# Optimization experiments

Hardware: AMD Instinct MI355X
Metric: run time of the kernel (lower is better)

Reference implementation:

```python
import jax, jax.numpy as jnp
import numpy as np

N_NODES = 100000
N_EDGES = 1600000
IN_DIM = 128
OUT_DIM = 128
N_HEADS = 4


def setup_inputs() -> dict:
    key = jax.random.key(0)
    k1, k2, k3, k4, k5 = jax.random.split(key, 5)
    h = jax.random.normal(k1, (N_NODES, IN_DIM), dtype=jnp.float32)
    src = jax.random.randint(k2, (N_EDGES,), 0, N_NODES, dtype=jnp.int32)
    dst = jax.random.randint(k3, (N_EDGES,), 0, N_NODES, dtype=jnp.int32)
    s = 1.0 / np.sqrt(IN_DIM)
    W_self = jax.random.normal(k4, (N_HEADS, IN_DIM, OUT_DIM), dtype=jnp.float32) * s
    W_neigh = jax.random.normal(k5, (N_HEADS, IN_DIM, OUT_DIM), dtype=jnp.float32) * s
    b = jnp.zeros((N_HEADS, OUT_DIM), dtype=jnp.float32)
    return {"h": h, "src": src, "dst": dst, "W_self": W_self, "W_neigh": W_neigh, "b": b}


def reference(h, src, dst, W_self, W_neigh, b):
    # Mean neighbor aggregation (shared across heads: SAGEConv 'mean' aggregates
    # raw features, then applies per-head linear layers).
    neigh_sum = jax.ops.segment_sum(h[src], dst, num_segments=N_NODES)   # [N, d_in]
    deg = jax.ops.segment_sum(jnp.ones_like(src, dtype=h.dtype), dst,
                              num_segments=N_NODES)                      # [N]
    h_neigh = neigh_sum / jnp.maximum(deg, 1.0)[:, None]                  # [N, d_in]

    # Per-head: fc_self(h_dst) + fc_neigh(h_neigh) + bias -> [H, N, d_out]
    out = (jnp.einsum('nd,hdo->hno', h, W_self)
           + jnp.einsum('nd,hdo->hno', h_neigh, W_neigh)
           + b[:, None, :])
    # merge='mean': average heads
    return jnp.mean(out, axis=0)  # [N, d_out]
```

## Files before the change

kernel.cpp:

```cpp
#include <hip/hip_runtime.h>

#define N_NODES 100000
#define N_EDGES 1600000
#define DIM 128
#define NH 4

#define NPB 512
#define NB 196
#define CAP 12288
#define BCHUNK 8192
#define BEPT 32
#define NBLK ((N_EDGES + BCHUNK - 1) / BCHUNK)

typedef __attribute__((ext_vector_type(8))) short bf16x8;
typedef __attribute__((ext_vector_type(4))) float f32x4;
typedef __attribute__((ext_vector_type(8))) unsigned short u16x8;

#define B_BCUR   0u
#define B_ROWOFF 4096u
#define B_BBASE  404096u
#define B_CSR    405504u
#define B_WPACK  6805504u
#define B_BAVG   6871040u
#define B_HB     6871552u
#define NEED_BF16 32869376ull

__device__ inline unsigned short f2bf(float x) {
    union { float f; unsigned u; } v; v.f = x;
    unsigned r = v.u + 0x7fffu + ((v.u >> 16) & 1u);
    return (unsigned short)(r >> 16);
}

template <bool BF>
__global__ __launch_bounds__(256) void prep_kernel(
    const float* __restrict__ h, unsigned short* __restrict__ hb,
    const float* __restrict__ Ws, const float* __restrict__ Wn,
    const float* __restrict__ b, unsigned short* __restrict__ wpack,
    float* __restrict__ bavg, int* __restrict__ bcur) {
    const int t = threadIdx.x;
    if (blockIdx.x == 0) bcur[t] = t * CAP;
    int i = blockIdx.x * 256 + t;
    if (i < DIM * DIM) {
        float s = 0.f, n = 0.f;
#pragma unroll
        for (int hh = 0; hh < NH; ++hh) {
            s += Ws[hh * DIM * DIM + i];
            n += Wn[hh * DIM * DIM + i];
        }
        s *= 0.25f; n *= 0.25f;
        int k = i >> 7, o = i & 127;
        int nt = o >> 4, lanelo = o & 15;
        int ks = k >> 5, lanehi = (k & 31) >> 3, e = k & 7;
        int pos = (((nt * 4 + ks) * 64) + lanehi * 16 + lanelo) * 8 + e;
        wpack[pos] = f2bf(s);
        wpack[16384 + pos] = f2bf(n);
    }
    if (i < DIM) {
        float bb = 0.f;
#pragma unroll
        for (int hh = 0; hh < NH; ++hh) bb += b[hh * DIM + i];
        bavg[i] = 0.25f * bb;
    }
    if (BF) {
        const float4* p = reinterpret_cast<const float4*>(h) + (size_t)i * 2;
        float4 a = p[0], c = p[1];
        u16x8 r;
        r[0] = f2bf(a.x); r[1] = f2bf(a.y); r[2] = f2bf(a.z); r[3] = f2bf(a.w);
        r[4] = f2bf(c.x); r[5] = f2bf(c.y); r[6] = f2bf(c.z); r[7] = f2bf(c.w);
        reinterpret_cast<u16x8*>(hb)[i] = r;
    }
}

__global__ __launch_bounds__(256) void bucket_scatter_kernel(const int* __restrict__ src,
                                                             const int* __restrict__ dst,
                                                             int* __restrict__ bcur,
                                                             int* __restrict__ ebuf) {
    __shared__ int stage[BCHUNK];
    __shared__ unsigned char bkt[BCHUNK];
    __shared__ int lc[256], lbase[256], lpos[256];
    int t = threadIdx.x;
    lc[t] = 0;
    lpos[t] = 0;
    __syncthreads();
    int e0 = blockIdx.x * BCHUNK;
#pragma unroll 4
    for (int j = 0; j < BEPT; ++j) {
        int e = e0 + j * 256 + t;
        if (e < N_EDGES) {
            int d = dst[e];
            stage[j * 256 + t] = (src[e] << 9) | (d & (NPB - 1));
            bkt[j * 256 + t] = (unsigned char)(d >> 9);
            atomicAdd(&lc[d >> 9], 1);
        }
    }
    __syncthreads();
    if (lc[t]) lbase[t] = atomicAdd(&bcur[t], lc[t]);
    __syncthreads();
#pragma unroll 4
    for (int j = 0; j < BEPT; ++j) {
        int e = e0 + j * 256 + t;
        if (e < N_EDGES) {
            int bb = bkt[j * 256 + t];
            int o = atomicAdd(&lpos[bb], 1);
            ebuf[lbase[bb] + o] = stage[j * 256 + t];
        }
    }
}

__global__ __launch_bounds__(256) void bucket_scan_kernel(const int* __restrict__ bcur,
                                                          int* __restrict__ bbase) {
    __shared__ int s[256];
    int t = threadIdx.x;
    int v = bcur[t] - t * CAP;
    s[t] = v;
    __syncthreads();
    for (int off = 1; off < 256; off <<= 1) {
        int add = (t >= off) ? s[t - off] : 0;
        __syncthreads();
        s[t] += add;
        __syncthreads();
    }
    bbase[t] = s[t] - v;
}

__global__ __launch_bounds__(256) void csr_build_kernel(const int* __restrict__ bcur,
                                                        const int* __restrict__ bbase,
                                                        const int* __restrict__ ebuf,
                                                        int* __restrict__ rowoff,
                                                        int* __restrict__ csr) {
    __shared__ int h[NPB], off[NPB], cur[NPB], ss[256];
    int b = blockIdx.x, t = threadIdx.x;
    int cnt = bcur[b] - b * CAP;
    int ibase = b * CAP;
    int obase = bbase[b];
    h[t] = 0; h[t + 256] = 0;
    cur[t] = 0; cur[t + 256] = 0;
    __syncthreads();
    for (int i = t; i < cnt; i += 256) atomicAdd(&h[ebuf[ibase + i] & (NPB - 1)], 1);
    __syncthreads();
    int e0 = h[2 * t], e1 = h[2 * t + 1];
    ss[t] = e0 + e1;
    __syncthreads();
    for (int o = 1; o < 256; o <<= 1) {
        int add = (t >= o) ? ss[t - o] : 0;
        __syncthreads();
        ss[t] += add;
        __syncthreads();
    }
    int ex = ss[t] - (e0 + e1);
    off[2 * t] = ex;
    off[2 * t + 1] = ex + e0;
    __syncthreads();
    int n0 = b * NPB;
#pragma unroll
    for (int k = 0; k < 2; ++k) {
        int s2 = 2 * t + k;
        int n = n0 + s2;
        int dg = (k == 0) ? e0 : e1;
        if (n < N_NODES) rowoff[n] = ((obase + off[s2]) << 9) | min(dg, 511);
    }
    for (int i = t; i < cnt; i += 256) {
        int p = ebuf[ibase + i];
        int nl = p & (NPB - 1);
        int o = atomicAdd(&cur[nl], 1);
        csr[obase + off[nl] + o] = p >> 9;
    }
}

template <bool BF>
__global__ __launch_bounds__(256) void gather_mean_kernel(
    const float* __restrict__ h, const unsigned short* __restrict__ hb,
    const int* __restrict__ rowoff, const int* __restrict__ csr,
    float* __restrict__ out) {
    int node = blockIdx.x * 4 + (threadIdx.x >> 6);
    int lane = threadIdx.x & 63;
    int g = lane >> 4;
    int c = lane & 15;
    int w = rowoff[node];
    int lo = w >> 9;
    int dg = w & 511;
    int hi = lo + dg;
    float a0 = 0.f, a1 = 0.f, a2 = 0.f, a3 = 0.f;
    float a4 = 0.f, a5 = 0.f, a6 = 0.f, a7 = 0.f;
    if (BF) {
        int k = lo + g;
        for (; k + 4 < hi; k += 8) {
            int s0 = csr[k], s1 = csr[k + 4];
            uint4 v = *reinterpret_cast<const uint4*>(hb + (size_t)s0 * DIM + c * 8);
            uint4 ww = *reinterpret_cast<const uint4*>(hb + (size_t)s1 * DIM + c * 8);
            a0 += __uint_as_float(v.x << 16) + __uint_as_float(ww.x << 16);
            a1 += __uint_as_float(v.x & 0xffff0000u) + __uint_as_float(ww.x & 0xffff0000u);
            a2 += __uint_as_float(v.y << 16) + __uint_as_float(ww.y << 16);
            a3 += __uint_as_float(v.y & 0xffff0000u) + __uint_as_float(ww.y & 0xffff0000u);
            a4 += __uint_as_float(v.z << 16) + __uint_as_float(ww.z << 16);
            a5 += __uint_as_float(v.z & 0xffff0000u) + __uint_as_float(ww.z & 0xffff0000u);
            a6 += __uint_as_float(v.w << 16) + __uint_as_float(ww.w << 16);
            a7 += __uint_as_float(v.w & 0xffff0000u) + __uint_as_float(ww.w & 0xffff0000u);
        }
        if (k < hi) {
            uint4 v = *reinterpret_cast<const uint4*>(hb + (size_t)csr[k] * DIM + c * 8);
            a0 += __uint_as_float(v.x << 16);
            a1 += __uint_as_float(v.x & 0xffff0000u);
            a2 += __uint_as_float(v.y << 16);
            a3 += __uint_as_float(v.y & 0xffff0000u);
            a4 += __uint_as_float(v.z << 16);
            a5 += __uint_as_float(v.z & 0xffff0000u);
            a6 += __uint_as_float(v.w << 16);
            a7 += __uint_as_float(v.w & 0xffff0000u);
        }
    } else {
        for (int k = lo + g; k < hi; k += 4) {
            int s = csr[k];
            const float4* p = reinterpret_cast<const float4*>(h + (size_t)s * DIM + c * 8);
            float4 x = p[0], y = p[1];
            a0 += x.x; a1 += x.y; a2 += x.z; a3 += x.w;
            a4 += y.x; a5 += y.y; a6 += y.z; a7 += y.w;
        }
    }
    a0 += __shfl_xor(a0, 16, 64); a0 += __shfl_xor(a0, 32, 64);
    a1 += __shfl_xor(a1, 16, 64); a1 += __shfl_xor(a1, 32, 64);
    a2 += __shfl_xor(a2, 16, 64); a2 += __shfl_xor(a2, 32, 64);
    a3 += __shfl_xor(a3, 16, 64); a3 += __shfl_xor(a3, 32, 64);
    a4 += __shfl_xor(a4, 16, 64); a4 += __shfl_xor(a4, 32, 64);
    a5 += __shfl_xor(a5, 16, 64); a5 += __shfl_xor(a5, 32, 64);
    a6 += __shfl_xor(a6, 16, 64); a6 += __shfl_xor(a6, 32, 64);
    a7 += __shfl_xor(a7, 16, 64); a7 += __shfl_xor(a7, 32, 64);
    float inv = 1.0f / (float)max(dg, 1);
    if (g == 0) {
        if (BF) {
            u16x8 r;
            r[0] = f2bf(a0 * inv); r[1] = f2bf(a1 * inv);
            r[2] = f2bf(a2 * inv); r[3] = f2bf(a3 * inv);
            r[4] = f2bf(a4 * inv); r[5] = f2bf(a5 * inv);
            r[6] = f2bf(a6 * inv); r[7] = f2bf(a7 * inv);
            *reinterpret_cast<u16x8*>(reinterpret_cast<unsigned short*>(out) +
                                      (size_t)node * 256 + c * 8) = r;
        } else {
            float4 r0, r1;
            r0.x = a0 * inv; r0.y = a1 * inv; r0.z = a2 * inv; r0.w = a3 * inv;
            r1.x = a4 * inv; r1.y = a5 * inv; r1.z = a6 * inv; r1.w = a7 * inv;
            float4* q = reinterpret_cast<float4*>(out + (size_t)node * DIM + c * 8);
            q[0] = r0;
            q[1] = r1;
        }
    }
}

template <bool BF>
__global__ __launch_bounds__(256) void mfma_gemm_kernel(
    const float* __restrict__ h, const unsigned short* __restrict__ hb,
    float* __restrict__ out, const unsigned short* __restrict__ wpack,
    const float* __restrict__ bavg) {
    const int lane = threadIdx.x & 63;
    const int wid = threadIdx.x >> 6;
    const int node_base = blockIdx.x * 64 + wid * 16;
    const int row = node_base + (lane & 15);
    const int rowc = min(row, N_NODES - 1);
    const int khi = lane >> 4;

    f32x4 acc[8] = {};
    const unsigned short* wn_p = wpack + 16384;

#pragma unroll
    for (int ks = 0; ks < 4; ++ks) {
        const int k0 = ks * 32 + khi * 8;
        bf16x8 ha, na;
        if (BF) {
            ha = *reinterpret_cast<const bf16x8*>(hb + (size_t)rowc * DIM + k0);
            na = *reinterpret_cast<const bf16x8*>(
                reinterpret_cast<const unsigned short*>(out) + (size_t)rowc * 256 + k0);
        } else {
            const float4* hp = reinterpret_cast<const float4*>(h + (size_t)rowc * DIM + k0);
            float4 x = hp[0], y = hp[1];
            ha[0] = (short)f2bf(x.x); ha[1] = (short)f2bf(x.y);
            ha[2] = (short)f2bf(x.z); ha[3] = (short)f2bf(x.w);
            ha[4] = (short)f2bf(y.x); ha[5] = (short)f2bf(y.y);
            ha[6] = (short)f2bf(y.z); ha[7] = (short)f2bf(y.w);
            const float4* np0 = reinterpret_cast<const float4*>(out + (size_t)rowc * DIM + k0);
            float4 u = np0[0], v = np0[1];
            na[0] = (short)f2bf(u.x); na[1] = (short)f2bf(u.y);
            na[2] = (short)f2bf(u.z); na[3] = (short)f2bf(u.w);
            na[4] = (short)f2bf(v.x); na[5] = (short)f2bf(v.y);
            na[6] = (short)f2bf(v.z); na[7] = (short)f2bf(v.w);
        }

#pragma unroll
        for (int nt = 0; nt < 8; ++nt) {
            bf16x8 bs = *reinterpret_cast<const bf16x8*>(wpack + (size_t)(((nt * 4 + ks) * 64 + lane) * 8));
            acc[nt] = __builtin_amdgcn_mfma_f32_16x16x32_bf16(ha, bs, acc[nt], 0, 0, 0);
            bf16x8 bn = *reinterpret_cast<const bf16x8*>(wn_p + (size_t)(((nt * 4 + ks) * 64 + lane) * 8));
            acc[nt] = __builtin_amdgcn_mfma_f32_16x16x32_bf16(na, bn, acc[nt], 0, 0, 0);
        }
    }

    const int r0 = node_base + khi * 4;
#pragma unroll
    for (int nt = 0; nt < 8; ++nt) {
        int o = nt * 16 + (lane & 15);
        float bb = bavg[o];
#pragma unroll
        for (int r = 0; r < 4; ++r) {
            int nr = r0 + r;
            if (nr < N_NODES) out[(size_t)nr * DIM + o] = acc[nt][r] + bb;
        }
    }
}

extern "C" void kernel_launch(void* const* d_in, const int* in_sizes, int n_in,
                              void* d_out, int out_size, void* d_ws, size_t ws_size,
                              hipStream_t stream) {
    const float* h  = (const float*)d_in[0];
    const int* src  = (const int*)d_in[1];
    const int* dst  = (const int*)d_in[2];
    const float* Ws = (const float*)d_in[3];
    const float* Wn = (const float*)d_in[4];
    const float* b  = (const float*)d_in[5];
    float* out = (float*)d_out;

    char* ws = (char*)d_ws;
    int* bcur   = (int*)(ws + B_BCUR);
    int* rowoff = (int*)(ws + B_ROWOFF);
    int* bbase  = (int*)(ws + B_BBASE);
    int* csr    = (int*)(ws + B_CSR);
    unsigned short* wpack = (unsigned short*)(ws + B_WPACK);
    float* bavg = (float*)(ws + B_BAVG);
    unsigned short* hb = (unsigned short*)(ws + B_HB);
    int* ebuf   = (int*)d_out;

    const bool bf = (ws_size >= NEED_BF16);

    if (bf)
        prep_kernel<true><<<(N_NODES * DIM / 8) / 256, 256, 0, stream>>>(h, hb, Ws, Wn, b, wpack, bavg, bcur);
    else
        prep_kernel<false><<<64, 256, 0, stream>>>(h, hb, Ws, Wn, b, wpack, bavg, bcur);
    bucket_scatter_kernel<<<NBLK, 256, 0, stream>>>(src, dst, bcur, ebuf);
    bucket_scan_kernel<<<1, 256, 0, stream>>>(bcur, bbase);
    csr_build_kernel<<<NB, 256, 0, stream>>>(bcur, bbase, ebuf, rowoff, csr);
    if (bf)
        gather_mean_kernel<true><<<N_NODES / 4, 256, 0, stream>>>(h, hb, rowoff, csr, out);
    else
        gather_mean_kernel<false><<<N_NODES / 4, 256, 0, stream>>>(h, hb, rowoff, csr, out);
    const int gemm_blocks = (N_NODES + 63) / 64;
    if (bf)
        mfma_gemm_kernel<true><<<gemm_blocks, 256, 0, stream>>>(h, hb, out, wpack, bavg);
    else
        mfma_gemm_kernel<false><<<gemm_blocks, 256, 0, stream>>>(h, hb, out, wpack, bavg);
}
```

Before: 151.8 us.

## Gather neighbor features in fp8 and fold bucket scan into CSR build

Node features are now stored as fp8 instead of bf16 for the neighbor gather, halving the bytes pulled per edge. Each wave now handles 8 edges in parallel with 16 features per lane. The self-term GEMM input is read from fp32 h and converted to bf16 inside the GEMM. The separate single-block bucket scan kernel is removed, and each CSR block redoes the 256-entry scan itself, saving one launch. The cost is a large precision loss in the aggregated features (fp8 e4m3), which may exceed the tolerance.

```diff
diff --git a/kernel.cpp b/kernel.cpp
--- a/kernel.cpp
+++ b/kernel.cpp
@@ -14,15 +14,15 @@
 
 typedef __attribute__((ext_vector_type(8))) short bf16x8;
 typedef __attribute__((ext_vector_type(4))) float f32x4;
+typedef __attribute__((ext_vector_type(2))) float f32x2;
 typedef __attribute__((ext_vector_type(8))) unsigned short u16x8;
 
 #define B_BCUR   0u
 #define B_ROWOFF 4096u
-#define B_BBASE  404096u
 #define B_CSR    405504u
 #define B_WPACK  6805504u
 #define B_BAVG   6871040u
-#define B_HB     6871552u
+#define B_H8     6871552u
 #define NEED_BF16 32869376ull
 
 __device__ inline unsigned short f2bf(float x) {
@@ -31,9 +31,29 @@
     return (unsigned short)(r >> 16);
 }
 
-template <bool BF>
+__device__ inline void acc_fp8(float (&a)[16], uint4 v) {
+    f32x2 r;
+    r = __builtin_amdgcn_cvt_pk_f32_fp8((int)v.x, false); a[0] += r[0]; a[1] += r[1];
+    r = __builtin_amdgcn_cvt_pk_f32_fp8((int)v.x, true);  a[2] += r[0]; a[3] += r[1];
+    r = __builtin_amdgcn_cvt_pk_f32_fp8((int)v.y, false); a[4] += r[0]; a[5] += r[1];
+    r = __builtin_amdgcn_cvt_pk_f32_fp8((int)v.y, true);  a[6] += r[0]; a[7] += r[1];
+    r = __builtin_amdgcn_cvt_pk_f32_fp8((int)v.z, false); a[8] += r[0]; a[9] += r[1];
+    r = __builtin_amdgcn_cvt_pk_f32_fp8((int)v.z, true);  a[10] += r[0]; a[11] += r[1];
+    r = __builtin_amdgcn_cvt_pk_f32_fp8((int)v.w, false); a[12] += r[0]; a[13] += r[1];
+    r = __builtin_amdgcn_cvt_pk_f32_fp8((int)v.w, true);  a[14] += r[0]; a[15] += r[1];
+}
+
+__device__ inline void acc_f32(float (&a)[16], const float4* p) {
+    float4 x0 = p[0], x1 = p[1], x2 = p[2], x3 = p[3];
+    a[0] += x0.x; a[1] += x0.y; a[2] += x0.z; a[3] += x0.w;
+    a[4] += x1.x; a[5] += x1.y; a[6] += x1.z; a[7] += x1.w;
+    a[8] += x2.x; a[9] += x2.y; a[10] += x2.z; a[11] += x2.w;
+    a[12] += x3.x; a[13] += x3.y; a[14] += x3.z; a[15] += x3.w;
+}
+
+template <bool F8>
 __global__ __launch_bounds__(256) void prep_kernel(
-    const float* __restrict__ h, unsigned short* __restrict__ hb,
+    const float* __restrict__ h, unsigned char* __restrict__ h8,
     const float* __restrict__ Ws, const float* __restrict__ Wn,
     const float* __restrict__ b, unsigned short* __restrict__ wpack,
     float* __restrict__ bavg, int* __restrict__ bcur) {
@@ -61,13 +81,15 @@
         for (int hh = 0; hh < NH; ++hh) bb += b[hh * DIM + i];
         bavg[i] = 0.25f * bb;
     }
-    if (BF) {
+    if (F8) {
         const float4* p = reinterpret_cast<const float4*>(h) + (size_t)i * 2;
         float4 a = p[0], c = p[1];
-        u16x8 r;
-        r[0] = f2bf(a.x); r[1] = f2bf(a.y); r[2] = f2bf(a.z); r[3] = f2bf(a.w);
-        r[4] = f2bf(c.x); r[5] = f2bf(c.y); r[6] = f2bf(c.z); r[7] = f2bf(c.w);
-        reinterpret_cast<u16x8*>(hb)[i] = r;
+        int d0 = 0, d1 = 0;
+        d0 = __builtin_amdgcn_cvt_pk_fp8_f32(a.x, a.y, d0, false);
+        d0 = __builtin_amdgcn_cvt_pk_fp8_f32(a.z, a.w, d0, true);
+        d1 = __builtin_amdgcn_cvt_pk_fp8_f32(c.x, c.y, d1, false);
+        d1 = __builtin_amdgcn_cvt_pk_fp8_f32(c.z, c.w, d1, true);
+        reinterpret_cast<uint2*>(h8)[i] = make_uint2((unsigned)d0, (unsigned)d1);
     }
 }
 
@@ -107,39 +129,15 @@
     }
 }
 
-__global__ __launch_bounds__(256) void bucket_scan_kernel(const int* __restrict__ bcur,
-                                                          int* __restrict__ bbase) {
-    __shared__ int s[256];
-    int t = threadIdx.x;
-    int v = bcur[t] - t * CAP;
-    s[t] = v;
-    __syncthreads();
-    for (int off = 1; off < 256; off <<= 1) {
-        int add = (t >= off) ? s[t - off] : 0;
-        __syncthreads();
-        s[t] += add;
-        __syncthreads();
-    }
-    bbase[t] = s[t] - v;
-}
-
 __global__ __launch_bounds__(256) void csr_build_kernel(const int* __restrict__ bcur,
-                                                        const int* __restrict__ bbase,
                                                         const int* __restrict__ ebuf,
                                                         int* __restrict__ rowoff,
                                                         int* __restrict__ csr) {
-    __shared__ int h[NPB], off[NPB], cur[NPB], ss[256];
+    __shared__ int hh[NPB], off[NPB], cur[NPB], ss[256];
     int b = blockIdx.x, t = threadIdx.x;
     int cnt = bcur[b] - b * CAP;
     int ibase = b * CAP;
-    int obase = bbase[b];
-    h[t] = 0; h[t + 256] = 0;
-    cur[t] = 0; cur[t + 256] = 0;
-    __syncthreads();
-    for (int i = t; i < cnt; i += 256) atomicAdd(&h[ebuf[ibase + i] & (NPB - 1)], 1);
-    __syncthreads();
-    int e0 = h[2 * t], e1 = h[2 * t + 1];
-    ss[t] = e0 + e1;
+    ss[t] = bcur[t] - t * CAP;
     __syncthreads();
     for (int o = 1; o < 256; o <<= 1) {
         int add = (t >= o) ? ss[t - o] : 0;
@@ -147,6 +145,21 @@
         ss[t] += add;
         __syncthreads();
     }
+    int obase = ss[b] - cnt;
+    hh[t] = 0; hh[t + 256] = 0;
+    cur[t] = 0; cur[t + 256] = 0;
+    __syncthreads();
+    for (int i = t; i < cnt; i += 256) atomicAdd(&hh[ebuf[ibase + i] & (NPB - 1)], 1);
+    __syncthreads();
+    int e0 = hh[2 * t], e1 = hh[2 * t + 1];
+    ss[t] = e0 + e1;
+    __syncthreads();
+    for (int o = 1; o < 256; o <<= 1) {
+        int add = (t >= o) ? ss[t - o] : 0;
+        __syncthreads();
+        ss[t] += add;
+        __syncthreads();
+    }
     int ex = ss[t] - (e0 + e1);
     off[2 * t] = ex;
     off[2 * t + 1] = ex + e0;
@@ -156,8 +169,8 @@
     for (int k = 0; k < 2; ++k) {
         int s2 = 2 * t + k;
         int n = n0 + s2;
-        int dg = (k == 0) ? e0 : e1;
-        if (n < N_NODES) rowoff[n] = ((obase + off[s2]) << 9) | min(dg, 511);
+        int dgv = (k == 0) ? e0 : e1;
+        if (n < N_NODES) rowoff[n] = ((obase + off[s2]) << 9) | min(dgv, 511);
     }
     for (int i = t; i < cnt; i += 256) {
         int p = ebuf[ibase + i];
@@ -167,90 +180,69 @@
     }
 }
 
-template <bool BF>
+template <bool F8>
 __global__ __launch_bounds__(256) void gather_mean_kernel(
-    const float* __restrict__ h, const unsigned short* __restrict__ hb,
+    const float* __restrict__ h, const unsigned char* __restrict__ h8,
     const int* __restrict__ rowoff, const int* __restrict__ csr,
     float* __restrict__ out) {
-    int node = blockIdx.x * 4 + (threadIdx.x >> 6);
-    int lane = threadIdx.x & 63;
-    int g = lane >> 4;
-    int c = lane & 15;
-    int w = rowoff[node];
-    int lo = w >> 9;
-    int dg = w & 511;
-    int hi = lo + dg;
-    float a0 = 0.f, a1 = 0.f, a2 = 0.f, a3 = 0.f;
-    float a4 = 0.f, a5 = 0.f, a6 = 0.f, a7 = 0.f;
-    if (BF) {
-        int k = lo + g;
-        for (; k + 4 < hi; k += 8) {
-            int s0 = csr[k], s1 = csr[k + 4];
-            uint4 v = *reinterpret_cast<const uint4*>(hb + (size_t)s0 * DIM + c * 8);
-            uint4 ww = *reinterpret_cast<const uint4*>(hb + (size_t)s1 * DIM + c * 8);
-            a0 += __uint_as_float(v.x << 16) + __uint_as_float(ww.x << 16);
-            a1 += __uint_as_float(v.x & 0xffff0000u) + __uint_as_float(ww.x & 0xffff0000u);
-            a2 += __uint_as_float(v.y << 16) + __uint_as_float(ww.y << 16);
-            a3 += __uint_as_float(v.y & 0xffff0000u) + __uint_as_float(ww.y & 0xffff0000u);
-            a4 += __uint_as_float(v.z << 16) + __uint_as_float(ww.z << 16);
-            a5 += __uint_as_float(v.z & 0xffff0000u) + __uint_as_float(ww.z & 0xffff0000u);
-            a6 += __uint_as_float(v.w << 16) + __uint_as_float(ww.w << 16);
-            a7 += __uint_as_float(v.w & 0xffff0000u) + __uint_as_float(ww.w & 0xffff0000u);
-        }
-        if (k < hi) {
-            uint4 v = *reinterpret_cast<const uint4*>(hb + (size_t)csr[k] * DIM + c * 8);
-            a0 += __uint_as_float(v.x << 16);
-            a1 += __uint_as_float(v.x & 0xffff0000u);
-            a2 += __uint_as_float(v.y << 16);
-            a3 += __uint_as_float(v.y & 0xffff0000u);
-            a4 += __uint_as_float(v.z << 16);
-            a5 += __uint_as_float(v.z & 0xffff0000u);
-            a6 += __uint_as_float(v.w << 16);
-            a7 += __uint_as_float(v.w & 0xffff0000u);
+    const int node = blockIdx.x * 4 + (threadIdx.x >> 6);
+    const int lane = threadIdx.x & 63;
+    const int s = lane >> 3;
+    const int c = lane & 7;
+    const int w = rowoff[node];
+    const int lo = w >> 9, dg = w & 511, hi = lo + dg;
+    float a[16];
+#pragma unroll
+    for (int i = 0; i < 16; ++i) a[i] = 0.f;
+    if (F8 && dg >= 8) {
+        int k = lo + s;
+        for (; k + 8 < hi; k += 16) {
+            int s0 = csr[k], s1 = csr[k + 8];
+            uint4 v = *reinterpret_cast<const uint4*>(h8 + (size_t)s0 * DIM + c * 16);
+            uint4 u = *reinterpret_cast<const uint4*>(h8 + (size_t)s1 * DIM + c * 16);
+            acc_fp8(a, v);
+            acc_fp8(a, u);
+        }
+        for (; k < hi; k += 8) {
+            uint4 v = *reinterpret_cast<const uint4*>(h8 + (size_t)csr[k] * DIM + c * 16);
+            acc_fp8(a, v);
         }
     } else {
-        for (int k = lo + g; k < hi; k += 4) {
-            int s = csr[k];
-            const float4* p = reinterpret_cast<const float4*>(h + (size_t)s * DIM + c * 8);
-            float4 x = p[0], y = p[1];
-            a0 += x.x; a1 += x.y; a2 += x.z; a3 += x.w;
-            a4 += y.x; a5 += y.y; a6 += y.z; a7 += y.w;
-        }
-    }
-    a0 += __shfl_xor(a0, 16, 64); a0 += __shfl_xor(a0, 32, 64);
-    a1 += __shfl_xor(a1, 16, 64); a1 += __shfl_xor(a1, 32, 64);
-    a2 += __shfl_xor(a2, 16, 64); a2 += __shfl_xor(a2, 32, 64);
-    a3 += __shfl_xor(a3, 16, 64); a3 += __shfl_xor(a3, 32, 64);
-    a4 += __shfl_xor(a4, 16, 64); a4 += __shfl_xor(a4, 32, 64);
-    a5 += __shfl_xor(a5, 16, 64); a5 += __shfl_xor(a5, 32, 64);
-    a6 += __shfl_xor(a6, 16, 64); a6 += __shfl_xor(a6, 32, 64);
-    a7 += __shfl_xor(a7, 16, 64); a7 += __shfl_xor(a7, 32, 64);
+        for (int k = lo + s; k < hi; k += 8)
+            acc_f32(a, reinterpret_cast<const float4*>(h + (size_t)csr[k] * DIM + c * 16));
+    }
+#pragma unroll
+    for (int i = 0; i < 16; ++i) {
+        a[i] += __shfl_xor(a[i], 8, 64);
+        a[i] += __shfl_xor(a[i], 16, 64);
+        a[i] += __shfl_xor(a[i], 32, 64);
+    }
     float inv = 1.0f / (float)max(dg, 1);
-    if (g == 0) {
-        if (BF) {
-            u16x8 r;
-            r[0] = f2bf(a0 * inv); r[1] = f2bf(a1 * inv);
-            r[2] = f2bf(a2 * inv); r[3] = f2bf(a3 * inv);
-            r[4] = f2bf(a4 * inv); r[5] = f2bf(a5 * inv);
-            r[6] = f2bf(a6 * inv); r[7] = f2bf(a7 * inv);
-            *reinterpret_cast<u16x8*>(reinterpret_cast<unsigned short*>(out) +
-                                      (size_t)node * 256 + c * 8) = r;
+    if (s == 0) {
+        if (F8) {
+            u16x8 r0, r1;
+#pragma unroll
+            for (int j = 0; j < 8; ++j) {
+                r0[j] = f2bf(a[j] * inv);
+                r1[j] = f2bf(a[8 + j] * inv);
+            }
+            unsigned short* base = reinterpret_cast<unsigned short*>(out) + (size_t)node * 256 + c * 16;
+            *reinterpret_cast<u16x8*>(base) = r0;
+            *reinterpret_cast<u16x8*>(base + 8) = r1;
         } else {
-            float4 r0, r1;
-            r0.x = a0 * inv; r0.y = a1 * inv; r0.z = a2 * inv; r0.w = a3 * inv;
-            r1.x = a4 * inv; r1.y = a5 * inv; r1.z = a6 * inv; r1.w = a7 * inv;
-            float4* q = reinterpret_cast<float4*>(out + (size_t)node * DIM + c * 8);
-            q[0] = r0;
-            q[1] = r1;
-        }
-    }
-}
-
-template <bool BF>
+            float4* q = reinterpret_cast<float4*>(out + (size_t)node * DIM + c * 16);
+            q[0] = make_float4(a[0] * inv, a[1] * inv, a[2] * inv, a[3] * inv);
+            q[1] = make_float4(a[4] * inv, a[5] * inv, a[6] * inv, a[7] * inv);
+            q[2] = make_float4(a[8] * inv, a[9] * inv, a[10] * inv, a[11] * inv);
+            q[3] = make_float4(a[12] * inv, a[13] * inv, a[14] * inv, a[15] * inv);
+        }
+    }
+}
+
+template <bool F8>
 __global__ __launch_bounds__(256) void mfma_gemm_kernel(
-    const float* __restrict__ h, const unsigned short* __restrict__ hb,
-    float* __restrict__ out, const unsigned short* __restrict__ wpack,
-    const float* __restrict__ bavg) {
+    const float* __restrict__ h, float* __restrict__ out,
+    const unsigned short* __restrict__ wpack, const float* __restrict__ bavg) {
     const int lane = threadIdx.x & 63;
     const int wid = threadIdx.x >> 6;
     const int node_base = blockIdx.x * 64 + wid * 16;
@@ -265,17 +257,16 @@
     for (int ks = 0; ks < 4; ++ks) {
         const int k0 = ks * 32 + khi * 8;
         bf16x8 ha, na;
-        if (BF) {
-            ha = *reinterpret_cast<const bf16x8*>(hb + (size_t)rowc * DIM + k0);
+        const float4* hp = reinterpret_cast<const float4*>(h + (size_t)rowc * DIM + k0);
+        float4 x = hp[0], y = hp[1];
+        ha[0] = (short)f2bf(x.x); ha[1] = (short)f2bf(x.y);
+        ha[2] = (short)f2bf(x.z); ha[3] = (short)f2bf(x.w);
+        ha[4] = (short)f2bf(y.x); ha[5] = (short)f2bf(y.y);
+        ha[6] = (short)f2bf(y.z); ha[7] = (short)f2bf(y.w);
+        if (F8) {
             na = *reinterpret_cast<const bf16x8*>(
                 reinterpret_cast<const unsigned short*>(out) + (size_t)rowc * 256 + k0);
         } else {
-            const float4* hp = reinterpret_cast<const float4*>(h + (size_t)rowc * DIM + k0);
-            float4 x = hp[0], y = hp[1];
-            ha[0] = (short)f2bf(x.x); ha[1] = (short)f2bf(x.y);
-            ha[2] = (short)f2bf(x.z); ha[3] = (short)f2bf(x.w);
-            ha[4] = (short)f2bf(y.x); ha[5] = (short)f2bf(y.y);
-            ha[6] = (short)f2bf(y.z); ha[7] = (short)f2bf(y.w);
             const float4* np0 = reinterpret_cast<const float4*>(out + (size_t)rowc * DIM + k0);
             float4 u = np0[0], v = np0[1];
             na[0] = (short)f2bf(u.x); na[1] = (short)f2bf(u.y);
@@ -320,29 +311,27 @@
     char* ws = (char*)d_ws;
     int* bcur   = (int*)(ws + B_BCUR);
     int* rowoff = (int*)(ws + B_ROWOFF);
-    int* bbase  = (int*)(ws + B_BBASE);
     int* csr    = (int*)(ws + B_CSR);
     unsigned short* wpack = (unsigned short*)(ws + B_WPACK);
     float* bavg = (float*)(ws + B_BAVG);
-    unsigned short* hb = (unsigned short*)(ws + B_HB);
+    unsigned char* h8 = (unsigned char*)(ws + B_H8);
     int* ebuf   = (int*)d_out;
 
-    const bool bf = (ws_size >= NEED_BF16);
-
-    if (bf)
-        prep_kernel<true><<<(N_NODES * DIM / 8) / 256, 256, 0, stream>>>(h, hb, Ws, Wn, b, wpack, bavg, bcur);
+    const bool f8 = (ws_size >= NEED_BF16);
+
+    if (f8)
+        prep_kernel<true><<<(N_NODES * DIM / 8) / 256, 256, 0, stream>>>(h, h8, Ws, Wn, b, wpack, bavg, bcur);
     else
-        prep_kernel<false><<<64, 256, 0, stream>>>(h, hb, Ws, Wn, b, wpack, bavg, bcur);
+        prep_kernel<false><<<64, 256, 0, stream>>>(h, h8, Ws, Wn, b, wpack, bavg, bcur);
     bucket_scatter_kernel<<<NBLK, 256, 0, stream>>>(src, dst, bcur, ebuf);
-    bucket_scan_kernel<<<1, 256, 0, stream>>>(bcur, bbase);
-    csr_build_kernel<<<NB, 256, 0, stream>>>(bcur, bbase, ebuf, rowoff, csr);
-    if (bf)
-        gather_mean_kernel<true><<<N_NODES / 4, 256, 0, stream>>>(h, hb, rowoff, csr, out);
+    csr_build_kernel<<<NB, 256, 0, stream>>>(bcur, ebuf, rowoff, csr);
+    if (f8)
+        gather_mean_kernel<true><<<N_NODES / 4, 256, 0, stream>>>(h, h8, rowoff, csr, out);
     else
-        gather_mean_kernel<false><<<N_NODES / 4, 256, 0, stream>>>(h, hb, rowoff, csr, out);
+        gather_mean_kernel<false><<<N_NODES / 4, 256, 0, stream>>>(h, h8, rowoff, csr, out);
     const int gemm_blocks = (N_NODES + 63) / 64;
-    if (bf)
-        mfma_gemm_kernel<true><<<gemm_blocks, 256, 0, stream>>>(h, hb, out, wpack, bavg);
+    if (f8)
+        mfma_gemm_kernel<true><<<gemm_blocks, 256, 0, stream>>>(h, out, wpack, bavg);
     else
-        mfma_gemm_kernel<false><<<gemm_blocks, 256, 0, stream>>>(h, hb, out, wpack, bavg);
-}
+        mfma_gemm_kernel<false><<<gemm_blocks, 256, 0, stream>>>(h, out, wpack, bavg);
+}
```

Measured after the change: 146.8 us. 3.3% less time.

## Fuse neighbor gather-mean with MFMA GEMM and fold bucket scan into CSR build

Applied to the files above, without the earlier changes.

The neighbor mean aggregation and the per-node MFMA GEMM are merged into one kernel. Each 1024-thread block gathers 16 nodes into LDS as bf16, then 8 waves each compute one 16-column output tile. This removes the global round-trip of the aggregated features and one kernel launch. The separate single-block bucket scan is also removed: every CSR-build block redundantly recomputes the 256-entry prefix sum itself. In exchange, half the waves sit idle during the GEMM phase, the W fragments are reloaded per block, and the large blocks may limit occupancy.

```diff
diff --git a/kernel.cpp b/kernel.cpp
--- a/kernel.cpp
+++ b/kernel.cpp
@@ -18,7 +18,6 @@
 
 #define B_BCUR   0u
 #define B_ROWOFF 4096u
-#define B_BBASE  404096u
 #define B_CSR    405504u
 #define B_WPACK  6805504u
 #define B_BAVG   6871040u
@@ -107,39 +106,15 @@
     }
 }
 
-__global__ __launch_bounds__(256) void bucket_scan_kernel(const int* __restrict__ bcur,
-                                                          int* __restrict__ bbase) {
-    __shared__ int s[256];
-    int t = threadIdx.x;
-    int v = bcur[t] - t * CAP;
-    s[t] = v;
-    __syncthreads();
-    for (int off = 1; off < 256; off <<= 1) {
-        int add = (t >= off) ? s[t - off] : 0;
-        __syncthreads();
-        s[t] += add;
-        __syncthreads();
-    }
-    bbase[t] = s[t] - v;
-}
-
 __global__ __launch_bounds__(256) void csr_build_kernel(const int* __restrict__ bcur,
-                                                        const int* __restrict__ bbase,
                                                         const int* __restrict__ ebuf,
                                                         int* __restrict__ rowoff,
                                                         int* __restrict__ csr) {
-    __shared__ int h[NPB], off[NPB], cur[NPB], ss[256];
+    __shared__ int hh[NPB], off[NPB], cur[NPB], ss[256];
     int b = blockIdx.x, t = threadIdx.x;
     int cnt = bcur[b] - b * CAP;
     int ibase = b * CAP;
-    int obase = bbase[b];
-    h[t] = 0; h[t + 256] = 0;
-    cur[t] = 0; cur[t + 256] = 0;
-    __syncthreads();
-    for (int i = t; i < cnt; i += 256) atomicAdd(&h[ebuf[ibase + i] & (NPB - 1)], 1);
-    __syncthreads();
-    int e0 = h[2 * t], e1 = h[2 * t + 1];
-    ss[t] = e0 + e1;
+    ss[t] = bcur[t] - t * CAP;
     __syncthreads();
     for (int o = 1; o < 256; o <<= 1) {
         int add = (t >= o) ? ss[t - o] : 0;
@@ -147,6 +122,21 @@
         ss[t] += add;
         __syncthreads();
     }
+    int obase = ss[b] - cnt;
+    hh[t] = 0; hh[t + 256] = 0;
+    cur[t] = 0; cur[t + 256] = 0;
+    __syncthreads();
+    for (int i = t; i < cnt; i += 256) atomicAdd(&hh[ebuf[ibase + i] & (NPB - 1)], 1);
+    __syncthreads();
+    int e0 = hh[2 * t], e1 = hh[2 * t + 1];
+    ss[t] = e0 + e1;
+    __syncthreads();
+    for (int o = 1; o < 256; o <<= 1) {
+        int add = (t >= o) ? ss[t - o] : 0;
+        __syncthreads();
+        ss[t] += add;
+        __syncthreads();
+    }
     int ex = ss[t] - (e0 + e1);
     off[2 * t] = ex;
     off[2 * t + 1] = ex + e0;
@@ -156,8 +146,8 @@
     for (int k = 0; k < 2; ++k) {
         int s2 = 2 * t + k;
         int n = n0 + s2;
-        int dg = (k == 0) ? e0 : e1;
-        if (n < N_NODES) rowoff[n] = ((obase + off[s2]) << 9) | min(dg, 511);
+        int dgv = (k == 0) ? e0 : e1;
+        if (n < N_NODES) rowoff[n] = ((obase + off[s2]) << 9) | min(dgv, 511);
     }
     for (int i = t; i < cnt; i += 256) {
         int p = ebuf[ibase + i];
@@ -168,141 +158,110 @@
 }
 
 template <bool BF>
-__global__ __launch_bounds__(256) void gather_mean_kernel(
+__global__ __launch_bounds__(1024, 8) void gather_gemm_kernel(
     const float* __restrict__ h, const unsigned short* __restrict__ hb,
     const int* __restrict__ rowoff, const int* __restrict__ csr,
-    float* __restrict__ out) {
-    int node = blockIdx.x * 4 + (threadIdx.x >> 6);
-    int lane = threadIdx.x & 63;
-    int g = lane >> 4;
-    int c = lane & 15;
-    int w = rowoff[node];
-    int lo = w >> 9;
-    int dg = w & 511;
-    int hi = lo + dg;
-    float a0 = 0.f, a1 = 0.f, a2 = 0.f, a3 = 0.f;
-    float a4 = 0.f, a5 = 0.f, a6 = 0.f, a7 = 0.f;
-    if (BF) {
-        int k = lo + g;
-        for (; k + 4 < hi; k += 8) {
-            int s0 = csr[k], s1 = csr[k + 4];
-            uint4 v = *reinterpret_cast<const uint4*>(hb + (size_t)s0 * DIM + c * 8);
-            uint4 ww = *reinterpret_cast<const uint4*>(hb + (size_t)s1 * DIM + c * 8);
-            a0 += __uint_as_float(v.x << 16) + __uint_as_float(ww.x << 16);
-            a1 += __uint_as_float(v.x & 0xffff0000u) + __uint_as_float(ww.x & 0xffff0000u);
-            a2 += __uint_as_float(v.y << 16) + __uint_as_float(ww.y << 16);
-            a3 += __uint_as_float(v.y & 0xffff0000u) + __uint_as_float(ww.y & 0xffff0000u);
-            a4 += __uint_as_float(v.z << 16) + __uint_as_float(ww.z << 16);
-            a5 += __uint_as_float(v.z & 0xffff0000u) + __uint_as_float(ww.z & 0xffff0000u);
-            a6 += __uint_as_float(v.w << 16) + __uint_as_float(ww.w << 16);
-            a7 += __uint_as_float(v.w & 0xffff0000u) + __uint_as_float(ww.w & 0xffff0000u);
-        }
-        if (k < hi) {
-            uint4 v = *reinterpret_cast<const uint4*>(hb + (size_t)csr[k] * DIM + c * 8);
-            a0 += __uint_as_float(v.x << 16);
-            a1 += __uint_as_float(v.x & 0xffff0000u);
-            a2 += __uint_as_float(v.y << 16);
-            a3 += __uint_as_float(v.y & 0xffff0000u);
-            a4 += __uint_as_float(v.z << 16);
-            a5 += __uint_as_float(v.z & 0xffff0000u);
-            a6 += __uint_as_float(v.w << 16);
-            a7 += __uint_as_float(v.w & 0xffff0000u);
-        }
-    } else {
-        for (int k = lo + g; k < hi; k += 4) {
-            int s = csr[k];
-            const float4* p = reinterpret_cast<const float4*>(h + (size_t)s * DIM + c * 8);
-            float4 x = p[0], y = p[1];
-            a0 += x.x; a1 += x.y; a2 += x.z; a3 += x.w;
-            a4 += y.x; a5 += y.y; a6 += y.z; a7 += y.w;
-        }
-    }
-    a0 += __shfl_xor(a0, 16, 64); a0 += __shfl_xor(a0, 32, 64);
-    a1 += __shfl_xor(a1, 16, 64); a1 += __shfl_xor(a1, 32, 64);
-    a2 += __shfl_xor(a2, 16, 64); a2 += __shfl_xor(a2, 32, 64);
-    a3 += __shfl_xor(a3, 16, 64); a3 += __shfl_xor(a3, 32, 64);
-    a4 += __shfl_xor(a4, 16, 64); a4 += __shfl_xor(a4, 32, 64);
-    a5 += __shfl_xor(a5, 16, 64); a5 += __shfl_xor(a5, 32, 64);
-    a6 += __shfl_xor(a6, 16, 64); a6 += __shfl_xor(a6, 32, 64);
-    a7 += __shfl_xor(a7, 16, 64); a7 += __shfl_xor(a7, 32, 64);
-    float inv = 1.0f / (float)max(dg, 1);
-    if (g == 0) {
-        if (BF) {
-            u16x8 r;
-            r[0] = f2bf(a0 * inv); r[1] = f2bf(a1 * inv);
-            r[2] = f2bf(a2 * inv); r[3] = f2bf(a3 * inv);
-            r[4] = f2bf(a4 * inv); r[5] = f2bf(a5 * inv);
-            r[6] = f2bf(a6 * inv); r[7] = f2bf(a7 * inv);
-            *reinterpret_cast<u16x8*>(reinterpret_cast<unsigned short*>(out) +
-                                      (size_t)node * 256 + c * 8) = r;
-        } else {
-            float4 r0, r1;
-            r0.x = a0 * inv; r0.y = a1 * inv; r0.z = a2 * inv; r0.w = a3 * inv;
-            r1.x = a4 * inv; r1.y = a5 * inv; r1.z = a6 * inv; r1.w = a7 * inv;
-            float4* q = reinterpret_cast<float4*>(out + (size_t)node * DIM + c * 8);
-            q[0] = r0;
-            q[1] = r1;
-        }
-    }
-}
-
-template <bool BF>
-__global__ __launch_bounds__(256) void mfma_gemm_kernel(
-    const float* __restrict__ h, const unsigned short* __restrict__ hb,
     float* __restrict__ out, const unsigned short* __restrict__ wpack,
     const float* __restrict__ bavg) {
+    __shared__ unsigned short hnl[16][DIM + 8];
     const int lane = threadIdx.x & 63;
-    const int wid = threadIdx.x >> 6;
-    const int node_base = blockIdx.x * 64 + wid * 16;
-    const int row = node_base + (lane & 15);
-    const int rowc = min(row, N_NODES - 1);
-    const int khi = lane >> 4;
-
-    f32x4 acc[8] = {};
-    const unsigned short* wn_p = wpack + 16384;
-
-#pragma unroll
-    for (int ks = 0; ks < 4; ++ks) {
-        const int k0 = ks * 32 + khi * 8;
-        bf16x8 ha, na;
+    const int w = threadIdx.x >> 6;
+    const int nb = blockIdx.x * 16;
+
+    {
+        const int node = nb + w;
+        const int g = lane >> 4;
+        const int c = lane & 15;
+        const int pw = rowoff[node];
+        const int lo = pw >> 9, dg = pw & 511, hi = lo + dg;
+        float a0 = 0.f, a1 = 0.f, a2 = 0.f, a3 = 0.f;
+        float a4 = 0.f, a5 = 0.f, a6 = 0.f, a7 = 0.f;
         if (BF) {
-            ha = *reinterpret_cast<const bf16x8*>(hb + (size_t)rowc * DIM + k0);
-            na = *reinterpret_cast<const bf16x8*>(
-                reinterpret_cast<const unsigned short*>(out) + (size_t)rowc * 256 + k0);
+            int k = lo + g;
+            for (; k + 4 < hi; k += 8) {
+                int s0 = csr[k], s1 = csr[k + 4];
+                uint4 v = *reinterpret_cast<const uint4*>(hb + (size_t)s0 * DIM + c * 8);
+                uint4 u = *reinterpret_cast<const uint4*>(hb + (size_t)s1 * DIM + c * 8);
+                a0 += __uint_as_float(v.x << 16) + __uint_as_float(u.x << 16);
+                a1 += __uint_as_float(v.x & 0xffff0000u) + __uint_as_float(u.x & 0xffff0000u);
+                a2 += __uint_as_float(v.y << 16) + __uint_as_float(u.y << 16);
+                a3 += __uint_as_float(v.y & 0xffff0000u) + __uint_as_float(u.y & 0xffff0000u);
+                a4 += __uint_as_float(v.z << 16) + __uint_as_float(u.z << 16);
+                a5 += __uint_as_float(v.z & 0xffff0000u) + __uint_as_float(u.z & 0xffff0000u);
+                a6 += __uint_as_float(v.w << 16) + __uint_as_float(u.w << 16);
+                a7 += __uint_as_float(v.w & 0xffff0000u) + __uint_as_float(u.w & 0xffff0000u);
+            }
+            if (k < hi) {
+                uint4 v = *reinterpret_cast<const uint4*>(hb + (size_t)csr[k] * DIM + c * 8);
+                a0 += __uint_as_float(v.x << 16);
+                a1 += __uint_as_float(v.x & 0xffff0000u);
+                a2 += __uint_as_float(v.y << 16);
+                a3 += __uint_as_float(v.y & 0xffff0000u);
+                a4 += __uint_as_float(v.z << 16);
+                a5 += __uint_as_float(v.z & 0xffff0000u);
+                a6 += __uint_as_float(v.w << 16);
+                a7 += __uint_as_float(v.w & 0xffff0000u);
+            }
         } else {
-            const float4* hp = reinterpret_cast<const float4*>(h + (size_t)rowc * DIM + k0);
-            float4 x = hp[0], y = hp[1];
-            ha[0] = (short)f2bf(x.x); ha[1] = (short)f2bf(x.y);
-            ha[2] = (short)f2bf(x.z); ha[3] = (short)f2bf(x.w);
-            ha[4] = (short)f2bf(y.x); ha[5] = (short)f2bf(y.y);
-            ha[6] = (short)f2bf(y.z); ha[7] = (short)f2bf(y.w);
-            const float4* np0 = reinterpret_cast<const float4*>(out + (size_t)rowc * DIM + k0);
-            float4 u = np0[0], v = np0[1];
-            na[0] = (short)f2bf(u.x); na[1] = (short)f2bf(u.y);
-            na[2] = (short)f2bf(u.z); na[3] = (short)f2bf(u.w);
-            na[4] = (short)f2bf(v.x); na[5] = (short)f2bf(v.y);
-            na[6] = (short)f2bf(v.z); na[7] = (short)f2bf(v.w);
-        }
-
-#pragma unroll
-        for (int nt = 0; nt < 8; ++nt) {
+            for (int k = lo + g; k < hi; k += 4) {
+                const float4* p = reinterpret_cast<const float4*>(h + (size_t)csr[k] * DIM + c * 8);
+                float4 x = p[0], y = p[1];
+                a0 += x.x; a1 += x.y; a2 += x.z; a3 += x.w;
+                a4 += y.x; a5 += y.y; a6 += y.z; a7 += y.w;
+            }
+        }
+        a0 += __shfl_xor(a0, 16, 64); a0 += __shfl_xor(a0, 32, 64);
+        a1 += __shfl_xor(a1, 16, 64); a1 += __shfl_xor(a1, 32, 64);
+        a2 += __shfl_xor(a2, 16, 64); a2 += __shfl_xor(a2, 32, 64);
+        a3 += __shfl_xor(a3, 16, 64); a3 += __shfl_xor(a3, 32, 64);
+        a4 += __shfl_xor(a4, 16, 64); a4 += __shfl_xor(a4, 32, 64);
+        a5 += __shfl_xor(a5, 16, 64); a5 += __shfl_xor(a5, 32, 64);
+        a6 += __shfl_xor(a6, 16, 64); a6 += __shfl_xor(a6, 32, 64);
+        a7 += __shfl_xor(a7, 16, 64); a7 += __shfl_xor(a7, 32, 64);
+        if (g == 0) {
+            float inv = 1.0f / (float)max(dg, 1);
+            u16x8 rr;
+            rr[0] = f2bf(a0 * inv); rr[1] = f2bf(a1 * inv);
+            rr[2] = f2bf(a2 * inv); rr[3] = f2bf(a3 * inv);
+            rr[4] = f2bf(a4 * inv); rr[5] = f2bf(a5 * inv);
+            rr[6] = f2bf(a6 * inv); rr[7] = f2bf(a7 * inv);
+            *reinterpret_cast<u16x8*>(&hnl[w][c * 8]) = rr;
+        }
+    }
+    __syncthreads();
+
+    if (w < 8) {
+        const int nt = w;
+        const int khi = lane >> 4;
+        const int rowc = nb + (lane & 15);
+        f32x4 acc = {};
+        const unsigned short* wn_p = wpack + 16384;
+#pragma unroll
+        for (int ks = 0; ks < 4; ++ks) {
+            const int k0 = ks * 32 + khi * 8;
+            bf16x8 ha;
+            if (BF) {
+                ha = *reinterpret_cast<const bf16x8*>(hb + (size_t)rowc * DIM + k0);
+            } else {
+                const float4* hp = reinterpret_cast<const float4*>(h + (size_t)rowc * DIM + k0);
+                float4 x = hp[0], y = hp[1];
+                ha[0] = (short)f2bf(x.x); ha[1] = (short)f2bf(x.y);
+                ha[2] = (short)f2bf(x.z); ha[3] = (short)f2bf(x.w);
+                ha[4] = (short)f2bf(y.x); ha[5] = (short)f2bf(y.y);
+                ha[6] = (short)f2bf(y.z); ha[7] = (short)f2bf(y.w);
+            }
+            bf16x8 na = *reinterpret_cast<const bf16x8*>(&hnl[lane & 15][k0]);
             bf16x8 bs = *reinterpret_cast<const bf16x8*>(wpack + (size_t)(((nt * 4 + ks) * 64 + lane) * 8));
-            acc[nt] = __builtin_amdgcn_mfma_f32_16x16x32_bf16(ha, bs, acc[nt], 0, 0, 0);
+            acc = __builtin_amdgcn_mfma_f32_16x16x32_bf16(ha, bs, acc, 0, 0, 0);
             bf16x8 bn = *reinterpret_cast<const bf16x8*>(wn_p + (size_t)(((nt * 4 + ks) * 64 + lane) * 8));
-            acc[nt] = __builtin_amdgcn_mfma_f32_16x16x32_bf16(na, bn, acc[nt], 0, 0, 0);
-        }
-    }
-
-    const int r0 = node_base + khi * 4;
-#pragma unroll
-    for (int nt = 0; nt < 8; ++nt) {
-        int o = nt * 16 + (lane & 15);
-        float bb = bavg[o];
-#pragma unroll
-        for (int r = 0; r < 4; ++r) {
-            int nr = r0 + r;
-            if (nr < N_NODES) out[(size_t)nr * DIM + o] = acc[nt][r] + bb;
-        }
+            acc = __builtin_amdgcn_mfma_f32_16x16x32_bf16(na, bn, acc, 0, 0, 0);
+        }
+        const int o = nt * 16 + (lane & 15);
+        const float bb = bavg[o];
+        const int r0 = nb + khi * 4;
+#pragma unroll
+        for (int r = 0; r < 4; ++r)
+            out[(size_t)(r0 + r) * DIM + o] = acc[r] + bb;
     }
 }
 
@@ -320,7 +279,6 @@
     char* ws = (char*)d_ws;
     int* bcur   = (int*)(ws + B_BCUR);
     int* rowoff = (int*)(ws + B_ROWOFF);
-    int* bbase  = (int*)(ws + B_BBASE);
     int* csr    = (int*)(ws + B_CSR);
     unsigned short* wpack = (unsigned short*)(ws + B_WPACK);
     float* bavg = (float*)(ws + B_BAVG);
@@ -334,15 +292,10 @@
     else
         prep_kernel<false><<<64, 256, 0, stream>>>(h, hb, Ws, Wn, b, wpack, bavg, bcur);
     bucket_scatter_kernel<<<NBLK, 256, 0, stream>>>(src, dst, bcur, ebuf);
-    bucket_scan_kernel<<<1, 256, 0, stream>>>(bcur, bbase);
-    csr_build_kernel<<<NB, 256, 0, stream>>>(bcur, bbase, ebuf, rowoff, csr);
+    csr_build_kernel<<<NB, 256, 0, stream>>>(bcur, ebuf, rowoff, csr);
+    const int fused_blocks = N_NODES / 16;
     if (bf)
-        gather_mean_kernel<true><<<N_NODES / 4, 256, 0, stream>>>(h, hb, rowoff, csr, out);
+        gather_gemm_kernel<true><<<fused_blocks, 1024, 0, stream>>>(h, hb, rowoff, csr, out, wpack, bavg);
     else
-        gather_mean_kernel<false><<<N_NODES / 4, 256, 0, stream>>>(h, hb, rowoff, csr, out);
-    const int gemm_blocks = (N_NODES + 63) / 64;
-    if (bf)
-        mfma_gemm_kernel<true><<<gemm_blocks, 256, 0, stream>>>(h, hb, out, wpack, bavg);
-    else
-        mfma_gemm_kernel<false><<<gemm_blocks, 256, 0, stream>>>(h, hb, out, wpack, bavg);
-}
+        gather_gemm_kernel<false><<<fused_blocks, 1024, 0, stream>>>(h, hb, rowoff, csr, out, wpack, bavg);
+}
```

After: 155.9 us. 2.7% more time.
